# Kernel optimization log

Measured on AMD Instinct MI355X. Metric: run time of the kernel, lower is better.

The kernel has to match this reference:

```python
import jax, jax.numpy as jnp
import numpy as np

T, IN, H, OUT = 4096, 2048, 2048, 1


def setup_inputs() -> dict:
    key = jax.random.key(0)
    ks = jax.random.split(key, 7)
    s = 0.02  # small init scale to keep gates in a sane range
    return {
        "x": jax.random.normal(ks[0], (T, 1, IN), dtype=jnp.float32),
        "W_ih": s * jax.random.normal(ks[1], (4 * H, IN), dtype=jnp.float32),
        "W_hh": s * jax.random.normal(ks[2], (4 * H, H), dtype=jnp.float32),
        "b_ih": s * jax.random.normal(ks[3], (4 * H,), dtype=jnp.float32),
        "b_hh": s * jax.random.normal(ks[4], (4 * H,), dtype=jnp.float32),
        "W_out": s * jax.random.normal(ks[5], (OUT, H), dtype=jnp.float32),
        "b_out": s * jax.random.normal(ks[6], (OUT,), dtype=jnp.float32),
    }


def reference(x, W_ih, W_hh, b_ih, b_hh, W_out, b_out):
    # Faithful LSTMCell loop (PyTorch gate order i, f, g, o) + per-step Linear.
    hidden = W_hh.shape[1]

    def step(carry, x_t):  # x_t: [1, IN]
        h, c = carry
        gates = x_t @ W_ih.T + b_ih + h @ W_hh.T + b_hh  # [1, 4H]
        i, f, g, o = jnp.split(gates, 4, axis=-1)
        i = jax.nn.sigmoid(i)
        f = jax.nn.sigmoid(f)
        g = jnp.tanh(g)
        o = jax.nn.sigmoid(o)
        c = f * c + i * g
        h = o * jnp.tanh(c)
        y = (h @ W_out.T + b_out)[0, 0]  # scalar, output_size == 1
        return (h, c), y

    h0 = jnp.zeros((1, hidden), dtype=x.dtype)
    c0 = jnp.zeros((1, hidden), dtype=x.dtype)
    _, res = jax.lax.scan(step, (h0, c0), x)
    return res  # [T]
```

## Files before the change

### kernel.cpp

```cpp
#include <hip/hip_runtime.h>

#define T_STEPS 4096
#define HD 2048
#define G4 8192
#define NWG 256
#define NTH 512
#define HSENT2 0xFF80FF80u

#define HB_OFF  131072
#define P_OFF   (131072 + 8192)
#define SMEM_BYTES (131072 + 8192 + 2048)

typedef __attribute__((ext_vector_type(8))) short bf16x8;
typedef __attribute__((ext_vector_type(4))) float f32x4;
typedef __attribute__((ext_vector_type(8))) unsigned short u16x8;

static __device__ __forceinline__ unsigned short f2bf(float f){
  union { float f; unsigned int u; } v; v.f = f;
  unsigned int r = (v.u + 0x7fffu + ((v.u >> 16) & 1u)) >> 16;
  return (unsigned short)r;
}
static __device__ __forceinline__ float bf2f(unsigned short s){
  union { unsigned int u; float f; } v; v.u = ((unsigned int)s) << 16;
  return v.f;
}
static __device__ __forceinline__ void st2_uc(unsigned short* p, unsigned int v){
  asm volatile("global_store_short %0, %1, off sc0 sc1" :: "v"(p), "v"(v) : "memory");
}

static __device__ __forceinline__ void poll_span(const unsigned int* ga, const unsigned int* gb,
                                                 unsigned la, unsigned lb, unsigned chk){
  unsigned t0, t1;
  asm volatile(
    "s_waitcnt vmcnt(0)\n\t"
    "s_mov_b32 m0, %[la]\n\t"
    "global_load_lds_dword %[ga], off sc0 sc1\n\t"
    "s_mov_b32 m0, %[lb]\n\t"
    "global_load_lds_dword %[gb], off sc0 sc1\n\t"
    "s_sleep 2\n\t"
    "s_mov_b32 m0, %[la]\n\t"
    "global_load_lds_dword %[ga], off sc0 sc1\n\t"
    "s_mov_b32 m0, %[lb]\n\t"
    "global_load_lds_dword %[gb], off sc0 sc1\n\t"
    "s_sleep 2\n\t"
    "s_mov_b32 m0, %[la]\n\t"
    "global_load_lds_dword %[ga], off sc0 sc1\n\t"
    "s_mov_b32 m0, %[lb]\n\t"
    "global_load_lds_dword %[gb], off sc0 sc1\n\t"
    "s_sleep 2\n\t"
    "s_mov_b32 m0, %[la]\n\t"
    "global_load_lds_dword %[ga], off sc0 sc1\n\t"
    "s_mov_b32 m0, %[lb]\n\t"
    "global_load_lds_dword %[gb], off sc0 sc1\n\t"
    "s_mov_b32 m0, -1\n\t"
    "Lpoll%=:\n\t"
    "s_waitcnt vmcnt(6)\n\t"
    "ds_read_b32 %[t0], %[chk]\n\t"
    "ds_read_b32 %[t1], %[chk] offset:256\n\t"
    "s_waitcnt lgkmcnt(0)\n\t"
    "v_xor_b32 %[t0], 0xff80ff80, %[t0]\n\t"
    "v_xor_b32 %[t1], 0xff80ff80, %[t1]\n\t"
    "v_min_u32 %[t0], %[t0], %[t1]\n\t"
    "v_cmp_eq_u32 vcc, 0, %[t0]\n\t"
    "s_cbranch_vccz Ldone%=\n\t"
    "s_mov_b32 m0, %[la]\n\t"
    "global_load_lds_dword %[ga], off sc0 sc1\n\t"
    "s_mov_b32 m0, %[lb]\n\t"
    "global_load_lds_dword %[gb], off sc0 sc1\n\t"
    "s_mov_b32 m0, -1\n\t"
    "s_sleep 2\n\t"
    "s_branch Lpoll%=\n\t"
    "Ldone%=:\n\t"
    : [t0]"=&v"(t0), [t1]"=&v"(t1)
    : [ga]"v"(ga), [gb]"v"(gb), [la]"s"(la), [lb]"s"(lb), [chk]"v"(chk)
    : "vcc", "memory");
}

__global__ void init_kernel(const float* __restrict__ b_ih, const float* __restrict__ b_hh,
                            float* __restrict__ bias, unsigned int* __restrict__ Hb32){
  int i = blockIdx.x*blockDim.x + threadIdx.x;
  int stride = gridDim.x*blockDim.x;
  const int HB_U32 = (T_STEPS+1)*HD/2;
  const int NTOT = G4 + HB_U32;
  for (int idx = i; idx < NTOT; idx += stride){
    if (idx < G4) bias[idx] = b_ih[idx] + b_hh[idx];
    else {
      int j = idx - G4;
      Hb32[j] = (j < HD/2) ? 0u : HSENT2;
    }
  }
}

__global__ __launch_bounds__(256) void gemm_xp(const float* __restrict__ X,
                                               const float* __restrict__ W,
                                               const float* __restrict__ bias,
                                               unsigned short* __restrict__ XP){
  __shared__ __align__(16) unsigned short As[128][40];
  __shared__ __align__(16) unsigned short Bs[128][40];
  const int tid = threadIdx.x;
  const int bx = blockIdx.x & 63;
  const int by = blockIdx.x >> 6;
  const int row0 = by*128, col0 = bx*128;
  const int l = tid & 63, w = tid >> 6;
  const int wrow = (w>>1)*64, wcol = (w&1)*64;
  const int lr = l & 15, lk = l >> 4;

  f32x4 acc[4][4];
  #pragma unroll
  for (int mi=0; mi<4; mi++)
    #pragma unroll
    for (int ni=0; ni<4; ni++)
      acc[mi][ni] = (f32x4){0.f,0.f,0.f,0.f};

  const int sr = tid >> 1;
  const int sh = (tid & 1) * 16;
  const float* xb = X + (size_t)(row0+sr)*2048 + sh;
  const float* wb = W + (size_t)(col0+sr)*2048 + sh;

  for (int k0 = 0; k0 < 2048; k0 += 32){
    __syncthreads();
    u16x8 va[2], vb[2];
    #pragma unroll
    for (int q=0; q<2; q++){
      float4 u = *(const float4*)(xb + k0 + q*8);
      float4 v = *(const float4*)(xb + k0 + q*8 + 4);
      u16x8 t;
      t[0]=f2bf(u.x); t[1]=f2bf(u.y); t[2]=f2bf(u.z); t[3]=f2bf(u.w);
      t[4]=f2bf(v.x); t[5]=f2bf(v.y); t[6]=f2bf(v.z); t[7]=f2bf(v.w);
      va[q]=t;
      float4 p = *(const float4*)(wb + k0 + q*8);
      float4 r = *(const float4*)(wb + k0 + q*8 + 4);
      u16x8 s;
      s[0]=f2bf(p.x); s[1]=f2bf(p.y); s[2]=f2bf(p.z); s[3]=f2bf(p.w);
      s[4]=f2bf(r.x); s[5]=f2bf(r.y); s[6]=f2bf(r.z); s[7]=f2bf(r.w);
      vb[q]=s;
    }
    *(u16x8*)&As[sr][sh]   = va[0];
    *(u16x8*)&As[sr][sh+8] = va[1];
    *(u16x8*)&Bs[sr][sh]   = vb[0];
    *(u16x8*)&Bs[sr][sh+8] = vb[1];
    __syncthreads();

    bf16x8 af[4], bfr[4];
    #pragma unroll
    for (int mi=0; mi<4; mi++) af[mi]  = *(const bf16x8*)&As[wrow+mi*16+lr][lk*8];
    #pragma unroll
    for (int ni=0; ni<4; ni++) bfr[ni] = *(const bf16x8*)&Bs[wcol+ni*16+lr][lk*8];
    #pragma unroll
    for (int mi=0; mi<4; mi++)
      #pragma unroll
      for (int ni=0; ni<4; ni++)
        acc[mi][ni] = __builtin_amdgcn_mfma_f32_16x16x32_bf16(af[mi], bfr[ni], acc[mi][ni], 0,0,0);
  }

  #pragma unroll
  for (int ni=0; ni<4; ni++){
    const int jc = col0 + wcol + ni*16 + lr;
    const float bv = bias[jc];
    #pragma unroll
    for (int mi=0; mi<4; mi++){
      const int tr0 = row0 + wrow + mi*16 + lk*4;
      #pragma unroll
      for (int r=0; r<4; r++)
        XP[(size_t)(tr0+r)*G4 + jc] = f2bf(acc[mi][ni][r] + bv);
    }
  }
}

__global__ __launch_bounds__(NTH, 1) void recur(const unsigned short* __restrict__ XP,
                                                const float* __restrict__ Whh,
                                                unsigned short* __restrict__ Hbuf){
  extern __shared__ char smem[];
  const int g = blockIdx.x;
  const int tid = threadIdx.x;
  const int l = tid & 63, w = tid >> 6;

  #pragma unroll
  for (int n=0; n<2; n++)
    #pragma unroll
    for (int kt=0; kt<8; kt++){
      const int rr = n*16 + (l & 15);
      const size_t jrow = (size_t)(rr>>3)*HD + (size_t)g*8 + (rr&7);
      const int k = w*256 + kt*32 + (l>>4)*8;
      const float* wp = Whh + jrow*HD + k;
      float4 fa = *(const float4*)wp;
      float4 fb = *(const float4*)(wp + 4);
      uint4 pk;
      pk.x = ((unsigned)f2bf(fa.y)<<16) | f2bf(fa.x);
      pk.y = ((unsigned)f2bf(fa.w)<<16) | f2bf(fa.z);
      pk.z = ((unsigned)f2bf(fb.y)<<16) | f2bf(fb.x);
      pk.w = ((unsigned)f2bf(fb.w)<<16) | f2bf(fb.z);
      *(uint4*)(smem + (size_t)(((w*16 + n*8 + kt)*64 + l)*16)) = pk;
    }
  __syncthreads();

  float c_reg = 0.f;
  float xpv = 0.f;
  if (w == 0 && l < 32)
    xpv = bf2f(XP[(size_t)(l>>3)*HD + (size_t)g*8 + (l&7)]);

  for (int t=0; t<T_STEPS; ++t){
    const int par = t & 1;
    {
      const unsigned int* hrow = (const unsigned int*)(Hbuf + (size_t)t*HD);
      const unsigned int* ga = hrow + w*128 + l;
      const unsigned int* gb = ga + 64;
      unsigned la = (unsigned)__builtin_amdgcn_readfirstlane(HB_OFF + par*4096 + w*512);
      unsigned lb = la + 256;
      unsigned chk = la + l*4;
      poll_span(ga, gb, la, lb, chk);
    }
    const char* hb = smem + HB_OFF + par*4096 + w*512;

    bf16x8 af[8];
    #pragma unroll
    for (int kt=0; kt<8; kt++)
      af[kt] = *(const bf16x8*)(hb + kt*64 + (l>>4)*16);

    f32x4 acc0 = (f32x4){0.f,0.f,0.f,0.f};
    f32x4 acc1 = (f32x4){0.f,0.f,0.f,0.f};
    #pragma unroll
    for (int kt=0; kt<8; kt++){
      bf16x8 b0 = *(const bf16x8*)(smem + (size_t)(((w*16 +     kt)*64 + l)*16));
      bf16x8 b1 = *(const bf16x8*)(smem + (size_t)(((w*16 + 8 + kt)*64 + l)*16));
      acc0 = __builtin_amdgcn_mfma_f32_16x16x32_bf16(af[kt], b0, acc0, 0,0,0);
      acc1 = __builtin_amdgcn_mfma_f32_16x16x32_bf16(af[kt], b1, acc1, 0,0,0);
    }
    float* part = (float*)(smem + P_OFF + par*1024);
    if (l < 16){
      part[l*8 + w]      = acc0[0];
      part[(16+l)*8 + w] = acc1[0];
    }
    __syncthreads();

    if (w == 0){
      __builtin_amdgcn_s_setprio(1);
      float act = 0.f;
      if (l < 32){
        float4 pa = *(const float4*)(part + l*8);
        float4 pb = *(const float4*)(part + l*8 + 4);
        float tot = ((pa.x+pa.y)+(pa.z+pa.w)) + ((pb.x+pb.y)+(pb.z+pb.w)) + xpv;
        const bool isg = ((l>>3) == 2);
        float z = __expf(isg ? -2.f*tot : -tot);
        float s = 1.f/(1.f + z);
        act = isg ? 2.f*s - 1.f : s;
      }
      float fv = __shfl_down(act, 8, 64);
      float gv = __shfl_down(act, 16, 64);
      float ov = __shfl_down(act, 24, 64);
      if (l < 8){
        c_reg = fv*c_reg + act*gv;
        float e2c = __expf(-2.f*c_reg);
        float th = (1.f - e2c)/(1.f + e2c);
        st2_uc(Hbuf + (size_t)(t+1)*HD + (size_t)g*8 + l, (unsigned)f2bf(ov*th));
      }
      __builtin_amdgcn_s_setprio(0);
      if (l < 32){
        const int tn = (t+1 < T_STEPS) ? t+1 : t;
        xpv = bf2f(XP[(size_t)tn*G4 + (size_t)(l>>3)*HD + (size_t)g*8 + (l&7)]);
      }
    }
  }
}

__global__ __launch_bounds__(256) void out_gemv(const unsigned short* __restrict__ Hbuf,
                                                const float* __restrict__ Wout,
                                                const float* __restrict__ bout,
                                                float* __restrict__ y){
  const int t = blockIdx.x;
  const int tid = threadIdx.x;
  u16x8 hv = *(const u16x8*)(Hbuf + (size_t)(t+1)*HD + tid*8);
  float4 w0 = *(const float4*)(Wout + tid*8);
  float4 w1 = *(const float4*)(Wout + tid*8 + 4);
  float s = bf2f(hv[0])*w0.x + bf2f(hv[1])*w0.y + bf2f(hv[2])*w0.z + bf2f(hv[3])*w0.w
          + bf2f(hv[4])*w1.x + bf2f(hv[5])*w1.y + bf2f(hv[6])*w1.z + bf2f(hv[7])*w1.w;
  #pragma unroll
  for (int off=32; off; off>>=1) s += __shfl_xor(s, off, 64);
  __shared__ float ps[4];
  if ((tid & 63) == 0) ps[tid>>6] = s;
  __syncthreads();
  if (tid == 0) y[t] = ps[0]+ps[1]+ps[2]+ps[3] + bout[0];
}

extern "C" void kernel_launch(void* const* d_in, const int* in_sizes, int n_in,
                              void* d_out, int out_size, void* d_ws, size_t ws_size,
                              hipStream_t stream) {
  const float* x    = (const float*)d_in[0];
  const float* Wih  = (const float*)d_in[1];
  const float* Whh  = (const float*)d_in[2];
  const float* b_ih = (const float*)d_in[3];
  const float* b_hh = (const float*)d_in[4];
  const float* Wout = (const float*)d_in[5];
  const float* bout = (const float*)d_in[6];
  float* y = (float*)d_out;

  char* ws = (char*)d_ws;
  unsigned short* XP   = (unsigned short*)(ws);
  unsigned short* Hbuf = (unsigned short*)(ws + 67108864);
  float* bias          = (float*)(ws + 83890176);

  init_kernel<<<2048, 256, 0, stream>>>(b_ih, b_hh, bias, (unsigned int*)Hbuf);
  gemm_xp<<<2048, 256, 0, stream>>>(x, Wih, bias, XP);

  hipFuncSetAttribute((const void*)recur,
                      hipFuncAttributeMaxDynamicSharedMemorySize, SMEM_BYTES);
  void* args[] = {(void*)&XP, (void*)&Whh, (void*)&Hbuf};
  hipLaunchCooperativeKernel((void*)recur, dim3(NWG), dim3(NTH), args,
                             SMEM_BYTES, stream);

  out_gemv<<<T_STEPS, 256, 0, stream>>>(Hbuf, Wout, bout, y);
}
```

Before: 11.36 ms.

## Replace async LDS-polling spin with register spin loads at device scope

The per-step wait for the previous hidden state used a batched asynchronous global-to-LDS poll with sleeps and a double-buffered LDS slot. It now spins on a direct global dwordx2 load into registers with device-scope (sc1) coherence, then writes the values to a single-buffered LDS slot owned by each wave. The hidden-state store also drops from system scope to device scope. The partial-sum layout is transposed so the reducing wave sums eight strided scalars instead of two float4s. The aim is to cut wake-up latency and coherence cost on the critical serial path, at the cost of a tighter spin that issues more memory traffic while waiting.

After: 10.28 ms. -9.5%, faster.

```diff
diff --git a/kernel.cpp b/kernel.cpp
--- a/kernel.cpp
+++ b/kernel.cpp
@@ -8,12 +8,13 @@
 #define HSENT2 0xFF80FF80u
 
 #define HB_OFF  131072
-#define P_OFF   (131072 + 8192)
-#define SMEM_BYTES (131072 + 8192 + 2048)
+#define P_OFF   (131072 + 4096)
+#define SMEM_BYTES (131072 + 4096 + 2048)
 
 typedef __attribute__((ext_vector_type(8))) short bf16x8;
 typedef __attribute__((ext_vector_type(4))) float f32x4;
 typedef __attribute__((ext_vector_type(8))) unsigned short u16x8;
+typedef __attribute__((ext_vector_type(2))) unsigned int u32x2;
 
 static __device__ __forceinline__ unsigned short f2bf(float f){
   union { float f; unsigned int u; } v; v.f = f;
@@ -24,56 +25,15 @@
   union { unsigned int u; float f; } v; v.u = ((unsigned int)s) << 16;
   return v.f;
 }
-static __device__ __forceinline__ void st2_uc(unsigned short* p, unsigned int v){
-  asm volatile("global_store_short %0, %1, off sc0 sc1" :: "v"(p), "v"(v) : "memory");
-}
-
-static __device__ __forceinline__ void poll_span(const unsigned int* ga, const unsigned int* gb,
-                                                 unsigned la, unsigned lb, unsigned chk){
-  unsigned t0, t1;
-  asm volatile(
-    "s_waitcnt vmcnt(0)\n\t"
-    "s_mov_b32 m0, %[la]\n\t"
-    "global_load_lds_dword %[ga], off sc0 sc1\n\t"
-    "s_mov_b32 m0, %[lb]\n\t"
-    "global_load_lds_dword %[gb], off sc0 sc1\n\t"
-    "s_sleep 2\n\t"
-    "s_mov_b32 m0, %[la]\n\t"
-    "global_load_lds_dword %[ga], off sc0 sc1\n\t"
-    "s_mov_b32 m0, %[lb]\n\t"
-    "global_load_lds_dword %[gb], off sc0 sc1\n\t"
-    "s_sleep 2\n\t"
-    "s_mov_b32 m0, %[la]\n\t"
-    "global_load_lds_dword %[ga], off sc0 sc1\n\t"
-    "s_mov_b32 m0, %[lb]\n\t"
-    "global_load_lds_dword %[gb], off sc0 sc1\n\t"
-    "s_sleep 2\n\t"
-    "s_mov_b32 m0, %[la]\n\t"
-    "global_load_lds_dword %[ga], off sc0 sc1\n\t"
-    "s_mov_b32 m0, %[lb]\n\t"
-    "global_load_lds_dword %[gb], off sc0 sc1\n\t"
-    "s_mov_b32 m0, -1\n\t"
-    "Lpoll%=:\n\t"
-    "s_waitcnt vmcnt(6)\n\t"
-    "ds_read_b32 %[t0], %[chk]\n\t"
-    "ds_read_b32 %[t1], %[chk] offset:256\n\t"
-    "s_waitcnt lgkmcnt(0)\n\t"
-    "v_xor_b32 %[t0], 0xff80ff80, %[t0]\n\t"
-    "v_xor_b32 %[t1], 0xff80ff80, %[t1]\n\t"
-    "v_min_u32 %[t0], %[t0], %[t1]\n\t"
-    "v_cmp_eq_u32 vcc, 0, %[t0]\n\t"
-    "s_cbranch_vccz Ldone%=\n\t"
-    "s_mov_b32 m0, %[la]\n\t"
-    "global_load_lds_dword %[ga], off sc0 sc1\n\t"
-    "s_mov_b32 m0, %[lb]\n\t"
-    "global_load_lds_dword %[gb], off sc0 sc1\n\t"
-    "s_mov_b32 m0, -1\n\t"
-    "s_sleep 2\n\t"
-    "s_branch Lpoll%=\n\t"
-    "Ldone%=:\n\t"
-    : [t0]"=&v"(t0), [t1]"=&v"(t1)
-    : [ga]"v"(ga), [gb]"v"(gb), [la]"s"(la), [lb]"s"(lb), [chk]"v"(chk)
-    : "vcc", "memory");
+
+static __device__ __forceinline__ u32x2 ld2_dev(const unsigned int* p){
+  u32x2 r;
+  asm volatile("global_load_dwordx2 %0, %1, off sc1\n\ts_waitcnt vmcnt(0)"
+               : "=v"(r) : "v"(p) : "memory");
+  return r;
+}
+static __device__ __forceinline__ void st2_dev(unsigned short* p, unsigned int v){
+  asm volatile("global_store_short %0, %1, off sc1" :: "v"(p), "v"(v) : "memory");
 }
 
 __global__ void init_kernel(const float* __restrict__ b_ih, const float* __restrict__ b_hh,
@@ -171,6 +131,7 @@
                                                 const float* __restrict__ Whh,
                                                 unsigned short* __restrict__ Hbuf){
   extern __shared__ char smem[];
+  char* hb = smem + HB_OFF;
   const int g = blockIdx.x;
   const int tid = threadIdx.x;
   const int l = tid & 63, w = tid >> 6;
@@ -200,22 +161,18 @@
     xpv = bf2f(XP[(size_t)(l>>3)*HD + (size_t)g*8 + (l&7)]);
 
   for (int t=0; t<T_STEPS; ++t){
-    const int par = t & 1;
+    u32x2 hv;
     {
-      const unsigned int* hrow = (const unsigned int*)(Hbuf + (size_t)t*HD);
-      const unsigned int* ga = hrow + w*128 + l;
-      const unsigned int* gb = ga + 64;
-      unsigned la = (unsigned)__builtin_amdgcn_readfirstlane(HB_OFF + par*4096 + w*512);
-      unsigned lb = la + 256;
-      unsigned chk = la + l*4;
-      poll_span(ga, gb, la, lb, chk);
-    }
-    const char* hb = smem + HB_OFF + par*4096 + w*512;
+      const unsigned int* hp = (const unsigned int*)(Hbuf + (size_t)t*HD) + w*128 + l*2;
+      do { hv = ld2_dev(hp); }
+      while (hv[0] == HSENT2 || hv[1] == HSENT2);
+    }
+    *(u32x2*)(hb + w*512 + l*8) = hv;
 
     bf16x8 af[8];
     #pragma unroll
     for (int kt=0; kt<8; kt++)
-      af[kt] = *(const bf16x8*)(hb + kt*64 + (l>>4)*16);
+      af[kt] = *(const bf16x8*)(hb + w*512 + kt*64 + (l>>4)*16);
 
     f32x4 acc0 = (f32x4){0.f,0.f,0.f,0.f};
     f32x4 acc1 = (f32x4){0.f,0.f,0.f,0.f};
@@ -226,10 +183,10 @@
       acc0 = __builtin_amdgcn_mfma_f32_16x16x32_bf16(af[kt], b0, acc0, 0,0,0);
       acc1 = __builtin_amdgcn_mfma_f32_16x16x32_bf16(af[kt], b1, acc1, 0,0,0);
     }
-    float* part = (float*)(smem + P_OFF + par*1024);
+    float* part = (float*)(smem + P_OFF) + (t&1)*256;
     if (l < 16){
-      part[l*8 + w]      = acc0[0];
-      part[(16+l)*8 + w] = acc1[0];
+      part[w*32 + l]      = acc0[0];
+      part[w*32 + 16 + l] = acc1[0];
     }
     __syncthreads();
 
@@ -237,9 +194,9 @@
       __builtin_amdgcn_s_setprio(1);
       float act = 0.f;
       if (l < 32){
-        float4 pa = *(const float4*)(part + l*8);
-        float4 pb = *(const float4*)(part + l*8 + 4);
-        float tot = ((pa.x+pa.y)+(pa.z+pa.w)) + ((pb.x+pb.y)+(pb.z+pb.w)) + xpv;
+        float tot = xpv;
+        #pragma unroll
+        for (int q=0; q<8; q++) tot += part[q*32 + l];
         const bool isg = ((l>>3) == 2);
         float z = __expf(isg ? -2.f*tot : -tot);
         float s = 1.f/(1.f + z);
@@ -252,7 +209,7 @@
         c_reg = fv*c_reg + act*gv;
         float e2c = __expf(-2.f*c_reg);
         float th = (1.f - e2c)/(1.f + e2c);
-        st2_uc(Hbuf + (size_t)(t+1)*HD + (size_t)g*8 + l, (unsigned)f2bf(ov*th));
+        st2_dev(Hbuf + (size_t)(t+1)*HD + (size_t)g*8 + l, (unsigned)f2bf(ov*th));
       }
       __builtin_amdgcn_s_setprio(0);
       if (l < 32){
```
